# Performance work log

Measured on AMD Instinct MI355X. Metric: run time of the kernel, lower is better.

Reference implementation:

```python
import jax, jax.numpy as jnp
import numpy as np

K = 3
P = K // 2


def _conv(x, w, b):
    y = jax.lax.conv_general_dilated(x, w, (1, 1), [(P, P), (P, P)],
                                     dimension_numbers=('NCHW', 'OIHW', 'NCHW'))
    return y + b[None, :, None, None]


def _deform_sample(x, py, px):
    # x: [B,C,H,W]; py,px: [B,KK,H,W] float sample coords -> [B,C,KK,H,W]
    B, C, H, W = x.shape
    xf = x.reshape(B, C, H * W)
    y0 = jnp.floor(py)
    x0 = jnp.floor(px)
    wy = py - y0
    wx = px - x0

    def corner(yi, xi, w):
        valid = (yi >= 0) & (yi < H) & (xi >= 0) & (xi < W)  # zero-pad outside
        idx = (jnp.clip(yi, 0, H - 1) * W + jnp.clip(xi, 0, W - 1)).astype(jnp.int32)
        g = jax.vmap(lambda xb, ib: xb[:, ib])(xf, idx)  # [B,C,KK,H,W]
        return g * (w * valid)[:, None]

    return (corner(y0, x0, (1 - wy) * (1 - wx)) + corner(y0, x0 + 1, (1 - wy) * wx)
            + corner(y0 + 1, x0, wy * (1 - wx)) + corner(y0 + 1, x0 + 1, wy * wx))


def setup_inputs() -> dict:
    key = jax.random.key(0)
    ks = jax.random.split(key, 8)
    B, C, H, W = 4, 256, 80, 80
    x = jax.random.normal(ks[0], (B, C, H, W), dtype=jnp.float32)
    offset_w = jax.random.normal(ks[1], (2 * K * K, C, K, K), dtype=jnp.float32) * 0.01
    offset_b = jax.random.normal(ks[2], (2 * K * K,), dtype=jnp.float32) * 0.01
    dcn_w = jax.random.normal(ks[3], (C, C, K, K), dtype=jnp.float32) * (1.0 / np.sqrt(C * K * K))
    gamma = jnp.ones((C,), jnp.float32)
    beta = jnp.zeros((C,), jnp.float32)
    mean = jax.random.normal(ks[4], (C,), dtype=jnp.float32) * 0.1
    var = jax.random.uniform(ks[5], (C,), dtype=jnp.float32, minval=0.5, maxval=1.5)
    return {'x': x, 'offset_w': offset_w, 'offset_b': offset_b, 'dcn_w': dcn_w,
            'gamma': gamma, 'beta': beta, 'mean': mean, 'var': var}


def reference(x, offset_w, offset_b, dcn_w, gamma, beta, mean, var):
    B, C, H, W = x.shape
    # offset conv -> [B, KK, 2(dy,dx), H, W] (torchvision DeformConv2d layout)
    off = _conv(x, offset_w, offset_b).reshape(B, K * K, 2, H, W)
    ki = jnp.repeat(jnp.arange(K), K).astype(x.dtype)  # kernel-tap row offset
    kj = jnp.tile(jnp.arange(K), K).astype(x.dtype)    # kernel-tap col offset
    hh = jnp.arange(H, dtype=x.dtype)
    ww = jnp.arange(W, dtype=x.dtype)
    py = off[:, :, 0] + (hh - P)[None, None, :, None] + ki[None, :, None, None]
    px = off[:, :, 1] + (ww - P)[None, None, None, :] + kj[None, :, None, None]
    vals = _deform_sample(x, py, px)                      # [B,C,KK,H,W]
    y = jnp.einsum('bckhw,ock->bohw', vals, dcn_w.reshape(C, C, K * K))
    # eval-mode BatchNorm + SiLU
    inv = jax.lax.rsqrt(var + 1e-5)
    y = (y - mean[None, :, None, None]) * (gamma * inv)[None, :, None, None] + beta[None, :, None, None]
    y = y * jax.nn.sigmoid(y)
    return x + y
```

## Files before the change

### kernel.cpp

```cpp
#include <hip/hip_runtime.h>
#include <math.h>
#include <stdint.h>

#define BATCH 4
#define CH    256
#define HH    80
#define WW    80
#define HW    (HH*WW)
#define NPIX  (BATCH*HW)
#define KK    9
#define CO    18
#define NCHUNK 72
#define NIV   36
#define PXB   64
#define NBLK  (NPIX/PXB)
#define AST   72

typedef _Float16 half8 __attribute__((ext_vector_type(8)));
typedef float    f32x4 __attribute__((ext_vector_type(4)));

__global__ __launch_bounds__(256) void k_transpose_x(const float* __restrict__ x,
                                                     _Float16* __restrict__ xt) {
    __shared__ float tile[32][33];
    int b  = blockIdx.z;
    int c0 = blockIdx.y * 32;
    int p0 = blockIdx.x * 32;
    int tx = threadIdx.x;
    int ty = threadIdx.y;
    const float* xb = x + (size_t)b * CH * HW;
    #pragma unroll
    for (int i = 0; i < 32; i += 8)
        tile[ty + i][tx] = xb[(size_t)(c0 + ty + i) * HW + p0 + tx];
    __syncthreads();
    _Float16* xtb = xt + (size_t)b * HW * CH;
    #pragma unroll
    for (int i = 0; i < 32; i += 8)
        xtb[(size_t)(p0 + ty + i) * CH + c0 + tx] = (_Float16)tile[tx][ty + i];
}

__global__ __launch_bounds__(256) void k_pack_all(const float* __restrict__ w,
                                                  const float* __restrict__ ow,
                                                  _Float16* __restrict__ wp,
                                                  _Float16* __restrict__ wpo) {
    int idx = blockIdx.x * 256 + threadIdx.x;
    if (idx < NIV * 16384) {
        int e    = idx & 7;
        int lane = (idx >> 3) & 63;
        int nn   = (idx >> 9) & 1;
        int ks   = (idx >> 10) & 1;
        int og   = (idx >> 11) & 7;
        int iv   = idx >> 14;
        int oc = og * 32 + nn * 16 + (lane & 15);
        int kl = ks * 32 + (lane >> 4) * 8 + e;
        int kg = iv * 64 + kl;
        int q  = kg >> 5;
        int tap = q >> 3;
        int c   = (q & 7) * 32 + (kg & 31);
        wp[idx] = (_Float16)w[((size_t)oc * CH + c) * KK + tap];
        return;
    }
    int idx2 = idx - NIV * 16384;
    if (idx2 >= NCHUNK * 1024) return;
    int e    = idx2 & 7;
    int lane = (idx2 >> 3) & 63;
    int nf   = (idx2 >> 9) & 1;
    int q    = idx2 >> 10;
    int oc  = nf * 16 + (lane & 15);
    int kic = (lane >> 4) * 8 + e;
    int tap = q >> 3;
    int c   = (q & 7) * 32 + kic;
    float v = (oc < CO) ? ow[((size_t)oc * CH + c) * KK + tap] : 0.f;
    wpo[idx2] = (_Float16)v;
}

#define BODY(IV, IVEND, BCUR, BNXT, RBUF, WBUF)                                    \
  {                                                                                \
    __syncthreads();                                                               \
    const int iv_ = (IV);                                                          \
    half8 pre[4]; float cwa[4];                                                    \
    if (iv_ < (IVEND) - 1) {                                                       \
      const _Float16* wb = wpk4 + (size_t)(iv_ + 1) * 16384 + og * 2048 + lane * 8;\
      BNXT[0] = *(const half8*)(wb);                                               \
      BNXT[1] = *(const half8*)(wb + 512);                                         \
      BNXT[2] = *(const half8*)(wb + 1024);                                        \
      BNXT[3] = *(const half8*)(wb + 1536);                                        \
      int chunk = 2 * (iv_ + 1) + sub;                                             \
      int tap = chunk >> 3, cg = chunk & 7;                                        \
      int4 ncb = cbl[gpx][tap]; float4 ncw = cwl[gpx][tap];                        \
      pre[0] = *(const half8*)(xtb + (size_t)ncb.x + cg * 32 + ko);                \
      pre[1] = *(const half8*)(xtb + (size_t)ncb.y + cg * 32 + ko);                \
      pre[2] = *(const half8*)(xtb + (size_t)ncb.z + cg * 32 + ko);                \
      pre[3] = *(const half8*)(xtb + (size_t)ncb.w + cg * 32 + ko);                \
      cwa[0] = ncw.x; cwa[1] = ncw.y; cwa[2] = ncw.z; cwa[3] = ncw.w;              \
    }                                                                              \
    __builtin_amdgcn_s_setprio(1);                                                 \
    _Pragma("unroll")                                                              \
    for (int mm = 0; mm < 4; ++mm) {                                               \
      half8 a0 = *(const half8*)&Ab[RBUF][(mm * 16 + lm) * AST + kg8];             \
      half8 a1 = *(const half8*)&Ab[RBUF][(mm * 16 + lm) * AST + 32 + kg8];        \
      acc[mm][0] = __builtin_amdgcn_mfma_f32_16x16x32_f16(a0, BCUR[0], acc[mm][0], 0, 0, 0); \
      acc[mm][1] = __builtin_amdgcn_mfma_f32_16x16x32_f16(a0, BCUR[1], acc[mm][1], 0, 0, 0); \
      acc[mm][0] = __builtin_amdgcn_mfma_f32_16x16x32_f16(a1, BCUR[2], acc[mm][0], 0, 0, 0); \
      acc[mm][1] = __builtin_amdgcn_mfma_f32_16x16x32_f16(a1, BCUR[3], acc[mm][1], 0, 0, 0); \
    }                                                                              \
    __builtin_amdgcn_s_setprio(0);                                                 \
    if (iv_ < (IVEND) - 1) {                                                       \
      half8 v = pre[0] * (_Float16)cwa[0];                                         \
      v += pre[1] * (_Float16)cwa[1];                                              \
      v += pre[2] * (_Float16)cwa[2];                                              \
      v += pre[3] * (_Float16)cwa[3];                                              \
      *(half8*)&Ab[WBUF][gpx * AST + cq * 8] = v;                                  \
    }                                                                              \
  }

__global__ __launch_bounds__(512, 4) void k_main(const float* __restrict__ x,
                                                 const _Float16* __restrict__ xt,
                                                 const _Float16* __restrict__ wpk4,
                                                 const _Float16* __restrict__ wopf,
                                                 const float* __restrict__ obias,
                                                 const float* __restrict__ gamma,
                                                 const float* __restrict__ beta,
                                                 const float* __restrict__ mean,
                                                 const float* __restrict__ var,
                                                 float* __restrict__ out) {
    __shared__ __align__(16) char pool[46080];
    _Float16 (*Ab)[PXB * AST] = (_Float16 (*)[PXB * AST])pool;
    int4   (*cbl)[KK] = (int4 (*)[KK])(pool + 18432);
    float4 (*cwl)[KK] = (float4 (*)[KK])(pool + 27648);
    float*  offl      = (float*)pool;

    int t = threadIdx.x, lane = t & 63, og = t >> 6;
    int lm = lane & 15, kg8 = (lane >> 4) * 8;
    int tile = ((int)blockIdx.x & 7) * (NBLK / 8) + ((int)blockIdx.x >> 3);
    int pixbase = tile * PXB;
    int bb = pixbase / HW, hw0 = pixbase % HW;
    const _Float16* xtb = xt + (size_t)bb * HW * CH;

    {
        int pxh = og & 1;
        int kq  = og >> 1;
        int apx0 = hw0 + pxh * 32 + lm;
        int apx1 = apx0 + 16;
        int h0 = apx0 / WW, w0 = apx0 % WW;
        int h1 = apx1 / WW, w1 = apx1 % WW;
        f32x4 oa0 = (f32x4)0.f, oa1 = (f32x4)0.f;
        f32x4 ob0 = (f32x4)0.f, ob1 = (f32x4)0.f;
        #pragma unroll
        for (int qq = 0; qq < 18; ++qq) {
            int q = kq * 18 + qq;
            int tap = q >> 3, cg = q & 7;
            int ki = tap / 3, kj = tap - ki * 3;
            int yy0 = h0 + ki - 1, xx0 = w0 + kj - 1;
            int yy1 = h1 + ki - 1, xx1 = w1 + kj - 1;
            bool ok0 = (yy0 >= 0) && (yy0 < HH) && (xx0 >= 0) && (xx0 < WW);
            bool ok1 = (yy1 >= 0) && (yy1 < HH) && (xx1 >= 0) && (xx1 < WW);
            half8 a0 = {0, 0, 0, 0, 0, 0, 0, 0};
            half8 a1 = {0, 0, 0, 0, 0, 0, 0, 0};
            if (ok0) a0 = *(const half8*)(xtb + (size_t)(yy0 * WW + xx0) * CH + cg * 32 + kg8);
            if (ok1) a1 = *(const half8*)(xtb + (size_t)(yy1 * WW + xx1) * CH + cg * 32 + kg8);
            const _Float16* wq = wopf + (size_t)q * 1024 + lane * 8;
            half8 b0 = *(const half8*)(wq);
            half8 b1 = *(const half8*)(wq + 512);
            oa0 = __builtin_amdgcn_mfma_f32_16x16x32_f16(a0, b0, oa0, 0, 0, 0);
            oa1 = __builtin_amdgcn_mfma_f32_16x16x32_f16(a0, b1, oa1, 0, 0, 0);
            ob0 = __builtin_amdgcn_mfma_f32_16x16x32_f16(a1, b0, ob0, 0, 0, 0);
            ob1 = __builtin_amdgcn_mfma_f32_16x16x32_f16(a1, b1, ob1, 0, 0, 0);
        }
        int prow = (lane >> 4) * 4;
        int r0 = (kq * PXB) + pxh * 32 + prow;
        int r1 = r0 + 16;
        #pragma unroll
        for (int r = 0; r < 4; ++r) {
            offl[(r0 + r) * CO + lm] = oa0[r];
            offl[(r1 + r) * CO + lm] = ob0[r];
        }
        if (lm < CO - 16) {
            #pragma unroll
            for (int r = 0; r < 4; ++r) {
                offl[(r0 + r) * CO + 16 + lm] = oa1[r];
                offl[(r1 + r) * CO + 16 + lm] = ob1[r];
            }
        }
    }
    __syncthreads();

    for (int task = t; task < PXB * KK; task += 512) {
        int p = task / KK, tap = task - (task / KK) * KK;
        float dy = obias[2 * tap], dx = obias[2 * tap + 1];
        #pragma unroll
        for (int ks = 0; ks < 4; ++ks) {
            dy += offl[((ks * PXB) + p) * CO + 2 * tap];
            dx += offl[((ks * PXB) + p) * CO + 2 * tap + 1];
        }
        int hw = hw0 + p, hc = hw / WW, wc = hw % WW;
        int ki = tap / 3, kj = tap - ki * 3;
        float py = dy + (float)(hc - 1 + ki);
        float px = dx + (float)(wc - 1 + kj);
        float y0f = floorf(py), x0f = floorf(px);
        float wy = py - y0f, wx = px - x0f;
        int y0 = (int)y0f, x0 = (int)x0f;
        int cb[4]; float cw[4];
        #pragma unroll
        for (int cy = 0; cy < 2; ++cy)
            #pragma unroll
            for (int cx = 0; cx < 2; ++cx) {
                int yy = y0 + cy, xx = x0 + cx;
                bool okc = (yy >= 0) && (yy < HH) && (xx >= 0) && (xx < WW);
                int yc = min(max(yy, 0), HH - 1);
                int xc = min(max(xx, 0), WW - 1);
                float wgt = (cy ? wy : 1.f - wy) * (cx ? wx : 1.f - wx);
                cb[cy * 2 + cx] = (yc * WW + xc) * CH;
                cw[cy * 2 + cx] = okc ? wgt : 0.f;
            }
        cbl[p][tap] = make_int4(cb[0], cb[1], cb[2], cb[3]);
        cwl[p][tap] = make_float4(cw[0], cw[1], cw[2], cw[3]);
    }
    __syncthreads();

    int gpx = t >> 3, cq = t & 7;
    int sub = cq >> 2, ko = (cq & 3) * 8;

    half8 bfA[4], bfB[4];
    {
        const _Float16* wb = wpk4 + og * 2048 + lane * 8;
        bfA[0] = *(const half8*)(wb);
        bfA[1] = *(const half8*)(wb + 512);
        bfA[2] = *(const half8*)(wb + 1024);
        bfA[3] = *(const half8*)(wb + 1536);
    }
    {
        int4 cb = cbl[gpx][0];
        float4 cw = cwl[gpx][0];
        int cg = sub;
        half8 v = *(const half8*)(xtb + (size_t)cb.x + cg * 32 + ko) * (_Float16)cw.x;
        v += *(const half8*)(xtb + (size_t)cb.y + cg * 32 + ko) * (_Float16)cw.y;
        v += *(const half8*)(xtb + (size_t)cb.z + cg * 32 + ko) * (_Float16)cw.z;
        v += *(const half8*)(xtb + (size_t)cb.w + cg * 32 + ko) * (_Float16)cw.w;
        *(half8*)&Ab[0][gpx * AST + cq * 8] = v;
    }

    f32x4 acc[4][2];
    #pragma unroll
    for (int mm = 0; mm < 4; ++mm) {
        acc[mm][0] = (f32x4)0.f;
        acc[mm][1] = (f32x4)0.f;
    }

    for (int ii = 0; ii < NIV; ii += 2) {
        BODY(ii,     NIV, bfA, bfB, 0, 1)
        BODY(ii + 1, NIV, bfB, bfA, 1, 0)
    }

    const float* xb2  = x   + (size_t)bb * CH * HW;
    float*       outb = out + (size_t)bb * CH * HW;
    #pragma unroll
    for (int nn = 0; nn < 2; ++nn) {
        int oc = og * 32 + nn * 16 + lm;
        float sc = gamma[oc] * rsqrtf(var[oc] + 1e-5f);
        float mn = mean[oc], bt = beta[oc];
        const float* xr   = xb2  + (size_t)oc * HW + hw0;
        float*       orow = outb + (size_t)oc * HW + hw0;
        #pragma unroll
        for (int mm = 0; mm < 4; ++mm) {
            int pb2 = mm * 16 + (lane >> 4) * 4;
            #pragma unroll
            for (int r = 0; r < 4; ++r) {
                float yv = (acc[mm][nn][r] - mn) * sc + bt;
                float s = yv * __builtin_amdgcn_rcpf(1.f + __expf(-yv));
                orow[pb2 + r] = xr[pb2 + r] + s;
            }
        }
    }
}

extern "C" void kernel_launch(void* const* d_in, const int* in_sizes, int n_in,
                              void* d_out, int out_size, void* d_ws, size_t ws_size,
                              hipStream_t stream) {
    const float* x        = (const float*)d_in[0];
    const float* offset_w = (const float*)d_in[1];
    const float* offset_b = (const float*)d_in[2];
    const float* dcn_w    = (const float*)d_in[3];
    const float* gamma    = (const float*)d_in[4];
    const float* beta     = (const float*)d_in[5];
    const float* mean     = (const float*)d_in[6];
    const float* var      = (const float*)d_in[7];
    float* out = (float*)d_out;

    _Float16* xt   = (_Float16*)d_ws;
    _Float16* wpk4 = xt + (size_t)NPIX * CH;
    _Float16* wopf = wpk4 + (size_t)NIV * 16384;

    k_transpose_x<<<dim3(HW / 32, CH / 32, BATCH), dim3(32, 8), 0, stream>>>(x, xt);
    k_pack_all<<<(NIV * 16384 + NCHUNK * 1024 + 255) / 256, 256, 0, stream>>>(dcn_w, offset_w, wpk4, wopf);
    k_main<<<NBLK, 512, 0, stream>>>(x, xt, wpk4, wopf, offset_b,
                                     gamma, beta, mean, var, out);
}
```

Before: 88.84 us.

## Halve main-loop barriers with two-stage LDS buffers and merge prep kernels

The main GEMM loop now runs 18 super-iterations, each consuming two K-slices from a 4-slot LDS ring. This halves the number of __syncthreads per block and interleaves weight loads and gather-blend writes between the two MFMA groups. Separately, the x transpose and the weight packing kernels are merged into one launch to save a kernel launch. LDS use grows from 45 KB to 54 KB per block, which may lower occupancy, and the prologue now stages two slices.

```diff
diff --git a/kernel.cpp b/kernel.cpp
--- a/kernel.cpp
+++ b/kernel.cpp
@@ -12,37 +12,41 @@
 #define CO    18
 #define NCHUNK 72
 #define NIV   36
+#define NSUP  18
 #define PXB   64
 #define NBLK  (NPIX/PXB)
 #define AST   72
+#define SUBSZ (PXB*AST)
 
 typedef _Float16 half8 __attribute__((ext_vector_type(8)));
 typedef float    f32x4 __attribute__((ext_vector_type(4)));
 
-__global__ __launch_bounds__(256) void k_transpose_x(const float* __restrict__ x,
-                                                     _Float16* __restrict__ xt) {
+#define TRN_BLOCKS 6400
+__global__ __launch_bounds__(256) void k_prep(const float* __restrict__ x,
+                                              _Float16* __restrict__ xt,
+                                              const float* __restrict__ w,
+                                              const float* __restrict__ ow,
+                                              _Float16* __restrict__ wp,
+                                              _Float16* __restrict__ wpo) {
     __shared__ float tile[32][33];
-    int b  = blockIdx.z;
-    int c0 = blockIdx.y * 32;
-    int p0 = blockIdx.x * 32;
-    int tx = threadIdx.x;
-    int ty = threadIdx.y;
-    const float* xb = x + (size_t)b * CH * HW;
-    #pragma unroll
-    for (int i = 0; i < 32; i += 8)
-        tile[ty + i][tx] = xb[(size_t)(c0 + ty + i) * HW + p0 + tx];
-    __syncthreads();
-    _Float16* xtb = xt + (size_t)b * HW * CH;
-    #pragma unroll
-    for (int i = 0; i < 32; i += 8)
-        xtb[(size_t)(p0 + ty + i) * CH + c0 + tx] = (_Float16)tile[tx][ty + i];
-}
-
-__global__ __launch_bounds__(256) void k_pack_all(const float* __restrict__ w,
-                                                  const float* __restrict__ ow,
-                                                  _Float16* __restrict__ wp,
-                                                  _Float16* __restrict__ wpo) {
-    int idx = blockIdx.x * 256 + threadIdx.x;
+    int bid = blockIdx.x;
+    if (bid < TRN_BLOCKS) {
+        int b  = bid / 1600;
+        int c0 = ((bid / 200) & 7) * 32;
+        int p0 = (bid % 200) * 32;
+        int tx = threadIdx.x & 31, ty = threadIdx.x >> 5;
+        const float* xb = x + (size_t)b * CH * HW;
+        #pragma unroll
+        for (int i = 0; i < 32; i += 8)
+            tile[ty + i][tx] = xb[(size_t)(c0 + ty + i) * HW + p0 + tx];
+        __syncthreads();
+        _Float16* xtb = xt + (size_t)b * HW * CH;
+        #pragma unroll
+        for (int i = 0; i < 32; i += 8)
+            xtb[(size_t)(p0 + ty + i) * CH + c0 + tx] = (_Float16)tile[tx][ty + i];
+        return;
+    }
+    int idx = (bid - TRN_BLOCKS) * 256 + threadIdx.x;
     if (idx < NIV * 16384) {
         int e    = idx & 7;
         int lane = (idx >> 3) & 63;
@@ -73,45 +77,39 @@
     wpo[idx2] = (_Float16)v;
 }
 
-#define BODY(IV, IVEND, BCUR, BNXT, RBUF, WBUF)                                    \
-  {                                                                                \
-    __syncthreads();                                                               \
-    const int iv_ = (IV);                                                          \
-    half8 pre[4]; float cwa[4];                                                    \
-    if (iv_ < (IVEND) - 1) {                                                       \
-      const _Float16* wb = wpk4 + (size_t)(iv_ + 1) * 16384 + og * 2048 + lane * 8;\
-      BNXT[0] = *(const half8*)(wb);                                               \
-      BNXT[1] = *(const half8*)(wb + 512);                                         \
-      BNXT[2] = *(const half8*)(wb + 1024);                                        \
-      BNXT[3] = *(const half8*)(wb + 1536);                                        \
-      int chunk = 2 * (iv_ + 1) + sub;                                             \
-      int tap = chunk >> 3, cg = chunk & 7;                                        \
-      int4 ncb = cbl[gpx][tap]; float4 ncw = cwl[gpx][tap];                        \
-      pre[0] = *(const half8*)(xtb + (size_t)ncb.x + cg * 32 + ko);                \
-      pre[1] = *(const half8*)(xtb + (size_t)ncb.y + cg * 32 + ko);                \
-      pre[2] = *(const half8*)(xtb + (size_t)ncb.z + cg * 32 + ko);                \
-      pre[3] = *(const half8*)(xtb + (size_t)ncb.w + cg * 32 + ko);                \
-      cwa[0] = ncw.x; cwa[1] = ncw.y; cwa[2] = ncw.z; cwa[3] = ncw.w;              \
-    }                                                                              \
-    __builtin_amdgcn_s_setprio(1);                                                 \
-    _Pragma("unroll")                                                              \
-    for (int mm = 0; mm < 4; ++mm) {                                               \
-      half8 a0 = *(const half8*)&Ab[RBUF][(mm * 16 + lm) * AST + kg8];             \
-      half8 a1 = *(const half8*)&Ab[RBUF][(mm * 16 + lm) * AST + 32 + kg8];        \
-      acc[mm][0] = __builtin_amdgcn_mfma_f32_16x16x32_f16(a0, BCUR[0], acc[mm][0], 0, 0, 0); \
-      acc[mm][1] = __builtin_amdgcn_mfma_f32_16x16x32_f16(a0, BCUR[1], acc[mm][1], 0, 0, 0); \
-      acc[mm][0] = __builtin_amdgcn_mfma_f32_16x16x32_f16(a1, BCUR[2], acc[mm][0], 0, 0, 0); \
-      acc[mm][1] = __builtin_amdgcn_mfma_f32_16x16x32_f16(a1, BCUR[3], acc[mm][1], 0, 0, 0); \
-    }                                                                              \
-    __builtin_amdgcn_s_setprio(0);                                                 \
-    if (iv_ < (IVEND) - 1) {                                                       \
-      half8 v = pre[0] * (_Float16)cwa[0];                                         \
-      v += pre[1] * (_Float16)cwa[1];                                              \
-      v += pre[2] * (_Float16)cwa[2];                                              \
-      v += pre[3] * (_Float16)cwa[3];                                              \
-      *(half8*)&Ab[WBUF][gpx * AST + cq * 8] = v;                                  \
-    }                                                                              \
-  }
+#define LOADB(DST, IV) { \
+    const _Float16* wb_ = wpk4 + (size_t)(IV) * 16384 + og * 2048 + lane * 8; \
+    DST[0] = *(const half8*)(wb_);        DST[1] = *(const half8*)(wb_ + 512); \
+    DST[2] = *(const half8*)(wb_ + 1024); DST[3] = *(const half8*)(wb_ + 1536); }
+
+#define LOADPRE(PRE, CWA, CHUNK) { \
+    int tap_ = (CHUNK) >> 3, cg_ = (CHUNK) & 7; \
+    int4 ncb_ = cbl[gpx][tap_]; float4 ncw_ = cwl[gpx][tap_]; \
+    PRE[0] = *(const half8*)(xtb + (size_t)ncb_.x + cg_ * 32 + ko); \
+    PRE[1] = *(const half8*)(xtb + (size_t)ncb_.y + cg_ * 32 + ko); \
+    PRE[2] = *(const half8*)(xtb + (size_t)ncb_.z + cg_ * 32 + ko); \
+    PRE[3] = *(const half8*)(xtb + (size_t)ncb_.w + cg_ * 32 + ko); \
+    CWA[0] = ncw_.x; CWA[1] = ncw_.y; CWA[2] = ncw_.z; CWA[3] = ncw_.w; }
+
+#define MFMA8(BASE, BF) { \
+    __builtin_amdgcn_s_setprio(1); \
+    _Pragma("unroll") \
+    for (int mm = 0; mm < 4; ++mm) { \
+      half8 a0 = *(const half8*)&(BASE)[(mm * 16 + lm) * AST + kg8]; \
+      half8 a1 = *(const half8*)&(BASE)[(mm * 16 + lm) * AST + 32 + kg8]; \
+      acc[mm][0] = __builtin_amdgcn_mfma_f32_16x16x32_f16(a0, BF[0], acc[mm][0], 0, 0, 0); \
+      acc[mm][1] = __builtin_amdgcn_mfma_f32_16x16x32_f16(a0, BF[1], acc[mm][1], 0, 0, 0); \
+      acc[mm][0] = __builtin_amdgcn_mfma_f32_16x16x32_f16(a1, BF[2], acc[mm][0], 0, 0, 0); \
+      acc[mm][1] = __builtin_amdgcn_mfma_f32_16x16x32_f16(a1, BF[3], acc[mm][1], 0, 0, 0); \
+    } \
+    __builtin_amdgcn_s_setprio(0); }
+
+#define BLEND(PRE, CWA, DSTBASE) { \
+    half8 v_ = PRE[0] * (_Float16)CWA[0]; \
+    v_ += PRE[1] * (_Float16)CWA[1]; \
+    v_ += PRE[2] * (_Float16)CWA[2]; \
+    v_ += PRE[3] * (_Float16)CWA[3]; \
+    *(half8*)&(DSTBASE)[gpx * AST + cq * 8] = v_; }
 
 __global__ __launch_bounds__(512, 4) void k_main(const float* __restrict__ x,
                                                  const _Float16* __restrict__ xt,
@@ -123,10 +121,10 @@
                                                  const float* __restrict__ mean,
                                                  const float* __restrict__ var,
                                                  float* __restrict__ out) {
-    __shared__ __align__(16) char pool[46080];
-    _Float16 (*Ab)[PXB * AST] = (_Float16 (*)[PXB * AST])pool;
-    int4   (*cbl)[KK] = (int4 (*)[KK])(pool + 18432);
-    float4 (*cwl)[KK] = (float4 (*)[KK])(pool + 27648);
+    __shared__ __align__(16) char pool[55296];
+    _Float16* AbF = (_Float16*)pool;
+    int4   (*cbl)[KK] = (int4 (*)[KK])(pool + 36864);
+    float4 (*cwl)[KK] = (float4 (*)[KK])(pool + 46080);
     float*  offl      = (float*)pool;
 
     int t = threadIdx.x, lane = t & 63, og = t >> 6;
@@ -221,13 +219,7 @@
     int sub = cq >> 2, ko = (cq & 3) * 8;
 
     half8 bfA[4], bfB[4];
-    {
-        const _Float16* wb = wpk4 + og * 2048 + lane * 8;
-        bfA[0] = *(const half8*)(wb);
-        bfA[1] = *(const half8*)(wb + 512);
-        bfA[2] = *(const half8*)(wb + 1024);
-        bfA[3] = *(const half8*)(wb + 1536);
-    }
+    LOADB(bfA, 0)
     {
         int4 cb = cbl[gpx][0];
         float4 cw = cwl[gpx][0];
@@ -236,7 +228,13 @@
         v += *(const half8*)(xtb + (size_t)cb.y + cg * 32 + ko) * (_Float16)cw.y;
         v += *(const half8*)(xtb + (size_t)cb.z + cg * 32 + ko) * (_Float16)cw.z;
         v += *(const half8*)(xtb + (size_t)cb.w + cg * 32 + ko) * (_Float16)cw.w;
-        *(half8*)&Ab[0][gpx * AST + cq * 8] = v;
+        *(half8*)&AbF[gpx * AST + cq * 8] = v;
+        int cg2 = 2 + sub;
+        half8 v2 = *(const half8*)(xtb + (size_t)cb.x + cg2 * 32 + ko) * (_Float16)cw.x;
+        v2 += *(const half8*)(xtb + (size_t)cb.y + cg2 * 32 + ko) * (_Float16)cw.y;
+        v2 += *(const half8*)(xtb + (size_t)cb.z + cg2 * 32 + ko) * (_Float16)cw.z;
+        v2 += *(const half8*)(xtb + (size_t)cb.w + cg2 * 32 + ko) * (_Float16)cw.w;
+        *(half8*)&AbF[SUBSZ + gpx * AST + cq * 8] = v2;
     }
 
     f32x4 acc[4][2];
@@ -246,9 +244,24 @@
         acc[mm][1] = (f32x4)0.f;
     }
 
-    for (int ii = 0; ii < NIV; ii += 2) {
-        BODY(ii,     NIV, bfA, bfB, 0, 1)
-        BODY(ii + 1, NIV, bfB, bfA, 1, 0)
+    for (int j = 0; j < NSUP; ++j) {
+        int rs = j & 1, ws = rs ^ 1;
+        _Float16* bufR0 = AbF + (rs * 2 + 0) * SUBSZ;
+        _Float16* bufR1 = AbF + (rs * 2 + 1) * SUBSZ;
+        _Float16* bufW0 = AbF + (ws * 2 + 0) * SUBSZ;
+        _Float16* bufW1 = AbF + (ws * 2 + 1) * SUBSZ;
+        bool gnext = (j < NSUP - 1);
+        __syncthreads();
+        LOADB(bfB, 2 * j + 1)
+        half8 pre0[4]; float cw0[4];
+        if (gnext) LOADPRE(pre0, cw0, 4 * j + 4 + sub)
+        MFMA8(bufR0, bfA)
+        if (gnext) BLEND(pre0, cw0, bufW0)
+        if (gnext) LOADB(bfA, 2 * j + 2)
+        half8 pre1[4]; float cw1[4];
+        if (gnext) LOADPRE(pre1, cw1, 4 * j + 6 + sub)
+        MFMA8(bufR1, bfB)
+        if (gnext) BLEND(pre1, cw1, bufW1)
     }
 
     const float* xb2  = x   + (size_t)bb * CH * HW;
@@ -290,8 +303,8 @@
     _Float16* wpk4 = xt + (size_t)NPIX * CH;
     _Float16* wopf = wpk4 + (size_t)NIV * 16384;
 
-    k_transpose_x<<<dim3(HW / 32, CH / 32, BATCH), dim3(32, 8), 0, stream>>>(x, xt);
-    k_pack_all<<<(NIV * 16384 + NCHUNK * 1024 + 255) / 256, 256, 0, stream>>>(dcn_w, offset_w, wpk4, wopf);
+    int prep_blocks = TRN_BLOCKS + (NIV * 16384 + NCHUNK * 1024 + 255) / 256;
+    k_prep<<<prep_blocks, 256, 0, stream>>>(x, xt, dcn_w, offset_w, wpk4, wopf);
     k_main<<<NBLK, 512, 0, stream>>>(x, xt, wpk4, wopf, offset_b,
                                      gamma, beta, mean, var, out);
 }
```

New measurement: 85.44 us. -3.8%, faster.
